# Optimization experiments

Hardware: AMD Instinct MI355X
Metric: run time of the kernel (lower is better)

The kernel has to match this reference:

```python
import jax, jax.numpy as jnp
import numpy as np

D_MODEL = 1024
NHEAD = 16
HEAD_DIM = D_MODEL // NHEAD
ROPE_BASE = 10000.0


def _rope_freq(T, head_dim):
    half = head_dim // 2
    pos = jnp.arange(T, dtype=jnp.float32)
    idx = jnp.arange(half, dtype=jnp.float32)
    freq_div = ROPE_BASE ** (2.0 * idx / head_dim)
    return pos[:, None] / freq_div[None, :]  # [T, half]


def _rope_rotate(x, cos, sin):
    # x: [B, H, T, d]; cos/sin: [T, d//2]
    half = x.shape[-1] // 2
    xl, xr = x[..., :half], x[..., half:]
    c = cos[None, None]
    s = sin[None, None]
    return jnp.concatenate([xl * c - xr * s, xl * s + xr * c], axis=-1)


def setup_inputs() -> dict:
    key = jax.random.key(0)
    ks = jax.random.split(key, 12)
    B, T = 2, 2048
    sd = 1.0 / np.sqrt(D_MODEL)
    inp = {
        "query": jax.random.normal(ks[0], (B, T, D_MODEL), jnp.float32),
        "key": jax.random.normal(ks[1], (B, T, D_MODEL), jnp.float32),
        "value": jax.random.normal(ks[2], (B, T, D_MODEL), jnp.float32),
        "frac": jax.random.uniform(ks[3], (B, T), jnp.float32),
        # Linear weights stored [in, out] (torch W.T)
        "Wq": jax.random.normal(ks[4], (D_MODEL, D_MODEL), jnp.float32) * sd,
        "Wk": jax.random.normal(ks[5], (D_MODEL, D_MODEL), jnp.float32) * sd,
        "Wv": jax.random.normal(ks[6], (D_MODEL, D_MODEL), jnp.float32) * sd,
        "Wo": jax.random.normal(ks[7], (D_MODEL, D_MODEL), jnp.float32) * sd,
        "bq": jnp.zeros((D_MODEL,), jnp.float32),
        "bk": jnp.zeros((D_MODEL,), jnp.float32),
        "bv": jnp.zeros((D_MODEL,), jnp.float32),
        "bo": jnp.zeros((D_MODEL,), jnp.float32),
        "alpha_pos": jax.random.normal(ks[8], (NHEAD,), jnp.float32) * 0.1,
        "alpha_neg": jax.random.normal(ks[9], (NHEAD,), jnp.float32) * 0.1,
    }
    return inp


def reference(query, key, value, frac, Wq, Wk, Wv, Wo, bq, bk, bv, bo, alpha_pos, alpha_neg):
    B, T, dm = query.shape
    H, hd = NHEAD, HEAD_DIM
    scale = hd ** -0.5

    def split_heads(x):  # [B,T,dm] -> [B,H,T,hd]
        return x.reshape(B, T, H, hd).transpose(0, 2, 1, 3)

    Q = split_heads(query @ Wq + bq)
    K = split_heads(key @ Wk + bk)
    V = split_heads(value @ Wv + bv)

    freq = _rope_freq(T, hd)
    cos, sin = jnp.cos(freq), jnp.sin(freq)
    Q = _rope_rotate(Q, cos, sin)
    K = _rope_rotate(K, cos, sin)

    scores = jnp.einsum("bhqd,bhkd->bhqk", Q, K) * scale  # [B,H,T,T]

    # data-dependent stoichiometric bias
    D = frac[:, None, :] - frac[:, :, None]  # [B,T,T], D[b,i,j] = frac_j - frac_i
    D_pos = jax.nn.relu(D)
    D_neg = -jax.nn.relu(-D)
    bias = (alpha_pos[None, :, None, None] * D_pos[:, None] +
            alpha_neg[None, :, None, None] * D_neg[:, None])  # [B,H,T,T]
    scores = scores + bias

    probs = jax.nn.softmax(scores, axis=-1)
    out = jnp.einsum("bhqk,bhkd->bhqd", probs, V)  # [B,H,T,hd]
    out = out.transpose(0, 2, 1, 3).reshape(B, T, dm)
    return out @ Wo + bo
```

## Files before the change

kernel.cpp:

```cpp
#include <hip/hip_runtime.h>


typedef unsigned short u16;
typedef __bf16 bf8v __attribute__((ext_vector_type(8)));
typedef __bf16 bf4v __attribute__((ext_vector_type(4)));
typedef float f32x4 __attribute__((ext_vector_type(4)));

#define D_MODEL 1024
#define T_SEQ   2048
#define NHEAD   16
#define HDIM    64
#define BATCH   2
#define M_TOT   (BATCH * T_SEQ)
#define LOG2E   1.4426950408889634f

__device__ __forceinline__ void gl2lds16(const u16* g, u16* l) {
  __builtin_amdgcn_global_load_lds(
      (__attribute__((address_space(1))) void*)g,
      (__attribute__((address_space(3))) void*)l, 16, 0, 0);
}

__global__ __launch_bounds__(256) void k_prep(
    const float* __restrict__ q, const float* __restrict__ k,
    const float* __restrict__ v, const float* __restrict__ Wq,
    const float* __restrict__ Wk, const float* __restrict__ Wv,
    const float* __restrict__ Wo, u16* __restrict__ Xb, u16* __restrict__ WtB,
    float* __restrict__ ct, float* __restrict__ st) {
  __shared__ float tile[64 * 65];
  int bx = blockIdx.x, tid = threadIdx.x;
  if (bx < 6144) {
    int z = bx >> 11, xb = bx & 2047;
    const float* src = (z == 0) ? q : (z == 1) ? k : v;
    u16* dst = Xb + (size_t)z * (M_TOT * D_MODEL);
    int idx = (xb * 256 + tid) * 8;
    float4 a = *(const float4*)(src + idx);
    float4 b = *(const float4*)(src + idx + 4);
    bf8v o;
    o[0] = (__bf16)a.x; o[1] = (__bf16)a.y; o[2] = (__bf16)a.z; o[3] = (__bf16)a.w;
    o[4] = (__bf16)b.x; o[5] = (__bf16)b.y; o[6] = (__bf16)b.z; o[7] = (__bf16)b.w;
    *(bf8v*)(dst + idx) = o;
  } else if (bx < 7168) {
    int idx2 = bx - 6144;
    int z = idx2 >> 8, rem = idx2 & 255;
    int k0 = (rem >> 4) * 64, n0 = (rem & 15) * 64;
    const float* W = (z == 0) ? Wq : (z == 1) ? Wk : (z == 2) ? Wv : Wo;
    u16* Wt = WtB + (size_t)z * (D_MODEL * D_MODEL);
#pragma unroll
    for (int i = 0; i < 16; i++) {
      int idx = tid + i * 256;
      int r = idx >> 6, c = idx & 63;
      tile[c * 65 + r] = W[(size_t)(k0 + r) * D_MODEL + n0 + c];
    }
    __syncthreads();
#pragma unroll
    for (int i = 0; i < 16; i++) {
      int idx = tid + i * 256;
      int r = idx >> 6, c = idx & 63;
      ((__bf16*)Wt)[(size_t)(n0 + r) * D_MODEL + k0 + c] = (__bf16)tile[r * 65 + c];
    }
  } else {
    int idx = (bx - 7168) * 256 + tid;
    int t = idx >> 5, d = idx & 31;
    float ang = (float)t * powf(10000.0f, -(float)d * (1.0f / 32.0f));
    ct[idx] = cosf(ang);
    st[idx] = sinf(ang);
  }
}

__device__ __forceinline__ void gemm_core_128(const u16* __restrict__ A,
                                              const u16* __restrict__ Bt,
                                              u16* sA, u16* sB,
                                              f32x4 (&acc)[4][4],
                                              int m0, int n0) {
  const int K = D_MODEL;
  int tid = threadIdx.x;
  int lane = tid & 63, wave = tid >> 6;
  int l15 = lane & 15, quad = lane >> 4;
  int wm = (wave >> 1) * 64, wn = (wave & 1) * 64;
  int r0 = tid >> 2, pcol0 = (tid & 3) * 8;
  int r1 = 64 + r0;
  const u16* A0 = A + (size_t)(m0 + r0) * K + pcol0;
  const u16* A1 = A + (size_t)(m0 + r1) * K + pcol0;
  const u16* B0 = Bt + (size_t)(n0 + r0) * K + pcol0;
  const u16* B1 = Bt + (size_t)(n0 + r1) * K + pcol0;
  u16* dA0 = sA + wave * 512;
  u16* dA1 = sA + 2048 + wave * 512;
  u16* dB0 = sB + wave * 512;
  u16* dB1 = sB + 2048 + wave * 512;
  for (int k0 = 0; k0 < K; k0 += 64) {
    __syncthreads();
    gl2lds16(A0 + k0, dA0);
    gl2lds16(A1 + k0, dA1);
    gl2lds16(A0 + k0 + 32, dA0 + 4096);
    gl2lds16(A1 + k0 + 32, dA1 + 4096);
    gl2lds16(B0 + k0, dB0);
    gl2lds16(B0 + k0 + 32, dB0 + 4096);
    gl2lds16(B1 + k0, dB1);
    gl2lds16(B1 + k0 + 32, dB1 + 4096);
    __syncthreads();
#pragma unroll
    for (int kh = 0; kh < 2; kh++) {
      bf8v af[4], bf[4];
#pragma unroll
      for (int i = 0; i < 4; i++)
        af[i] = *(const bf8v*)(sA + kh * 4096 + (wm + i * 16 + l15) * 32 + quad * 8);
#pragma unroll
      for (int i = 0; i < 4; i++)
        bf[i] = *(const bf8v*)(sB + kh * 4096 + (wn + i * 16 + l15) * 32 + quad * 8);
#pragma unroll
      for (int mi = 0; mi < 4; mi++)
#pragma unroll
        for (int ni = 0; ni < 4; ni++)
          acc[mi][ni] = __builtin_amdgcn_mfma_f32_16x16x32_bf16(
              af[mi], bf[ni], acc[mi][ni], 0, 0, 0);
    }
  }
}

__global__ __launch_bounds__(256) void k_gemm_qkv(
    const u16* __restrict__ Xb, const u16* __restrict__ WtB,
    const float* __restrict__ bq, const float* __restrict__ bk,
    const float* __restrict__ bv, const float* __restrict__ ctab,
    const float* __restrict__ stab, u16* __restrict__ OutB,
    u16* __restrict__ Vb) {
  __shared__ __align__(16) u16 sA[128 * 64];
  __shared__ __align__(16) u16 sB[128 * 64];
  int z = blockIdx.z;
  const u16* A = Xb + (size_t)z * (M_TOT * D_MODEL);
  const u16* Bt = WtB + (size_t)z * (D_MODEL * D_MODEL);
  const float* bias = (z == 0) ? bq : (z == 1) ? bk : bv;
  u16* Out = OutB + (size_t)z * (M_TOT * D_MODEL);
  int m0 = blockIdx.y * 128, n0 = blockIdx.x * 128;
  f32x4 acc[4][4] = {};
  gemm_core_128(A, Bt, sA, sB, acc, m0, n0);

  int tid = threadIdx.x, lane = tid & 63, wave = tid >> 6;
  int l15 = lane & 15, quad = lane >> 4;
  int wm = (wave >> 1) * 64, wn = (wave & 1) * 64;
  float bvv[4];
#pragma unroll
  for (int ni = 0; ni < 4; ni++) bvv[ni] = bias[n0 + wn + ni * 16 + l15];

  if (z < 2) {
    float qs = (z == 0) ? 0.125f * LOG2E : 1.0f;
#pragma unroll
    for (int mi = 0; mi < 4; mi++) {
#pragma unroll
      for (int r = 0; r < 4; r++) {
        int m = m0 + wm + mi * 16 + quad * 4 + r;
        size_t ro = (size_t)m * D_MODEL + n0 + wn;
        int tl = m & (T_SEQ - 1);
#pragma unroll
        for (int ni = 0; ni < 2; ni++) {
          int d = ni * 16 + l15;
          float c = ctab[tl * 32 + d], s = stab[tl * 32 + d];
          float xl = acc[mi][ni][r] + bvv[ni];
          float xr = acc[mi][ni + 2][r] + bvv[ni + 2];
          ((__bf16*)Out)[ro + d] = (__bf16)((xl * c - xr * s) * qs);
          ((__bf16*)Out)[ro + d + 32] = (__bf16)((xl * s + xr * c) * qs);
        }
      }
    }
  } else {
    int hh = (n0 + wn) >> 6;
    int mbase = m0 + wm;
    int bb = mbase >> 11;
    int tbase = mbase & (T_SEQ - 1);
    u16* Vw = Vb + (size_t)(bb * NHEAD + hh) * HDIM * T_SEQ;
#pragma unroll
    for (int mi = 0; mi < 4; mi++)
#pragma unroll
      for (int r = 0; r < 4; r++) {
        int t = tbase + mi * 16 + quad * 4 + r;
#pragma unroll
        for (int ni = 0; ni < 4; ni++) {
          int d = ni * 16 + l15;
          ((__bf16*)Vw)[(size_t)d * T_SEQ + t] = (__bf16)(acc[mi][ni][r] + bvv[ni]);
        }
      }
  }
}

__global__ __launch_bounds__(256) void k_gemm_out(
    const u16* __restrict__ ctx, const u16* __restrict__ Wot,
    const float* __restrict__ bo, float* __restrict__ Cout) {
  __shared__ __align__(16) u16 sA[64 * 64];
  __shared__ __align__(16) u16 sB[64 * 64];
  const int K = D_MODEL;
  int m0 = blockIdx.y * 64, n0 = blockIdx.x * 64;
  int tid = threadIdx.x, lane = tid & 63, wave = tid >> 6;
  int l15 = lane & 15, quad = lane >> 4;
  int wm = (wave >> 1) * 32, wn = (wave & 1) * 32;
  int r0 = tid >> 2, pcol0 = (tid & 3) * 8;
  const u16* A0 = ctx + (size_t)(m0 + r0) * K + pcol0;
  const u16* B0 = Wot + (size_t)(n0 + r0) * K + pcol0;
  u16* dA = sA + wave * 512;
  u16* dB = sB + wave * 512;
  f32x4 acc[2][2] = {};
  for (int k0 = 0; k0 < K; k0 += 64) {
    __syncthreads();
    gl2lds16(A0 + k0, dA);
    gl2lds16(A0 + k0 + 32, dA + 2048);
    gl2lds16(B0 + k0, dB);
    gl2lds16(B0 + k0 + 32, dB + 2048);
    __syncthreads();
#pragma unroll
    for (int kh = 0; kh < 2; kh++) {
      bf8v af[2], bf[2];
#pragma unroll
      for (int i = 0; i < 2; i++)
        af[i] = *(const bf8v*)(sA + kh * 2048 + (wm + i * 16 + l15) * 32 + quad * 8);
#pragma unroll
      for (int i = 0; i < 2; i++)
        bf[i] = *(const bf8v*)(sB + kh * 2048 + (wn + i * 16 + l15) * 32 + quad * 8);
#pragma unroll
      for (int mi = 0; mi < 2; mi++)
#pragma unroll
        for (int ni = 0; ni < 2; ni++)
          acc[mi][ni] = __builtin_amdgcn_mfma_f32_16x16x32_bf16(
              af[mi], bf[ni], acc[mi][ni], 0, 0, 0);
    }
  }
  float bvv[2];
#pragma unroll
  for (int ni = 0; ni < 2; ni++) bvv[ni] = bo[n0 + wn + ni * 16 + l15];
#pragma unroll
  for (int mi = 0; mi < 2; mi++)
#pragma unroll
    for (int r = 0; r < 4; r++) {
      size_t ro = (size_t)(m0 + wm + mi * 16 + quad * 4 + r) * D_MODEL + n0 + wn;
#pragma unroll
      for (int ni = 0; ni < 2; ni++)
        Cout[ro + ni * 16 + l15] = acc[mi][ni][r] + bvv[ni];
    }
}

__global__ __launch_bounds__(256) void k_attn(
    const u16* __restrict__ Qr, const u16* __restrict__ Kr,
    const u16* __restrict__ Vb, const float* __restrict__ frac,
    const float* __restrict__ alpha_pos, const float* __restrict__ alpha_neg,
    u16* __restrict__ ctx) {
  __shared__ __align__(16) u16 kT[2][64 * 64];
  __shared__ __align__(16) u16 vT[2][64 * 64];
  __shared__ __align__(16) u16 pT[4][2][16 * 72];
  int bh = blockIdx.y, b = bh >> 4, h = bh & 15;
  int q0 = blockIdx.x * 128;
  int tid = threadIdx.x, wave = tid >> 6, lane = tid & 63;
  int l15 = lane & 15, quad = lane >> 4;

  const u16* Kh = Kr + (size_t)b * T_SEQ * D_MODEL + h * HDIM;
  const u16* Vh = Vb + (size_t)bh * HDIM * T_SEQ;
  const float* fb = frac + b * T_SEQ;

  bf8v qf[2][2];
  float fq[2];
#pragma unroll
  for (int g = 0; g < 2; g++) {
    int qrow = q0 + wave * 32 + g * 16 + l15;
    const u16* qbase =
        Qr + (size_t)(b * T_SEQ + qrow) * D_MODEL + h * HDIM + quad * 8;
    qf[g][0] = *(const bf8v*)qbase;
    qf[g][1] = *(const bf8v*)(qbase + 32);
    fq[g] = fb[qrow];
  }
  float ap = alpha_pos[h] * LOG2E, an = alpha_neg[h] * LOG2E;
  bf8v onesv;
#pragma unroll
  for (int j = 0; j < 8; j++) onesv[j] = (__bf16)1.0f;
  f32x4 o[2][4] = {};
  f32x4 o_l[2] = {};
  u16* pw = &pT[wave][0][0];

  int x0 = (quad ^ (l15 & 7)) * 8;
  int kidx[4], vidx[4];
#pragma unroll
  for (int nt = 0; nt < 4; nt++) kidx[nt] = ((nt * 16 + l15) << 6) + x0;
#pragma unroll
  for (int dt = 0; dt < 4; dt++) vidx[dt] = ((dt * 16 + l15) << 6) + x0;
  int pidx = l15 * 72 + quad * 8;

  int p0 = tid, p1 = 256 + tid;
  int kr0 = p0 >> 3, gc0 = (p0 & 7) ^ (kr0 & 7);
  int kr1 = p1 >> 3, gc1 = (p1 & 7) ^ (kr1 & 7);
  const u16* kg0 = Kh + (size_t)kr0 * D_MODEL + gc0 * 8;
  const u16* kg1 = Kh + (size_t)kr1 * D_MODEL + gc1 * 8;
  const u16* vg0 = Vh + (size_t)kr0 * T_SEQ + gc0 * 8;
  const u16* vg1 = Vh + (size_t)kr1 * T_SEQ + gc1 * 8;
  int woff = wave * 512;

  auto stage = [&](int buf, int kbase) {
    gl2lds16(kg0 + (size_t)kbase * D_MODEL, kT[buf] + woff);
    gl2lds16(kg1 + (size_t)kbase * D_MODEL, kT[buf] + 2048 + woff);
    gl2lds16(vg0 + kbase, vT[buf] + woff);
    gl2lds16(vg1 + kbase, vT[buf] + 2048 + woff);
  };

  stage(0, 0);
  __syncthreads();

  for (int kt = 0; kt < T_SEQ / 64; kt++) {
    int kbase = kt * 64;
    int buf = kt & 1;
    if (kt + 1 < T_SEQ / 64) stage(buf ^ 1, kbase + 64);
    const u16* kb = kT[buf];
    const u16* vb = vT[buf];

    bf8v kf0[4], kf1[4];
#pragma unroll
    for (int nt = 0; nt < 4; nt++) {
      kf0[nt] = *(const bf8v*)(kb + kidx[nt]);
      kf1[nt] = *(const bf8v*)(kb + (kidx[nt] ^ 32));
    }
    bf8v vf[2][4];
#pragma unroll
    for (int dt = 0; dt < 4; dt++) {
      vf[0][dt] = *(const bf8v*)(vb + vidx[dt]);
      vf[1][dt] = *(const bf8v*)(vb + (vidx[dt] ^ 32));
    }
    f32x4 fk4[4];
#pragma unroll
    for (int nt = 0; nt < 4; nt++)
      fk4[nt] = *(const f32x4*)(fb + kbase + nt * 16 + quad * 4);

#pragma unroll
    for (int g = 0; g < 2; g++) {
      float fqg = fq[g];
      u16* pwg = pw + g * (16 * 72);
#pragma unroll
      for (int nt = 0; nt < 4; nt++) {
        f32x4 s = {};
        s = __builtin_amdgcn_mfma_f32_16x16x32_bf16(kf0[nt], qf[g][0], s, 0, 0, 0);
        s = __builtin_amdgcn_mfma_f32_16x16x32_bf16(kf1[nt], qf[g][1], s, 0, 0, 0);
        bf4v pk;
#pragma unroll
        for (int r = 0; r < 4; r++) {
          float dd = fk4[nt][r] - fqg;
          float sel = (dd >= 0.0f) ? ap : an;
          pk[r] = (__bf16)__builtin_amdgcn_exp2f(fmaf(dd, sel, s[r]));
        }
        *(bf4v*)(pwg + l15 * 72 + nt * 16 + quad * 4) = pk;
      }
      asm volatile("s_waitcnt lgkmcnt(0)" ::: "memory");
#pragma unroll
      for (int kc = 0; kc < 2; kc++) {
        bf8v pf = *(const bf8v*)(pwg + pidx + kc * 32);
        o_l[g] = __builtin_amdgcn_mfma_f32_16x16x32_bf16(pf, onesv, o_l[g], 0, 0, 0);
#pragma unroll
        for (int dt = 0; dt < 4; dt++)
          o[g][dt] = __builtin_amdgcn_mfma_f32_16x16x32_bf16(pf, vf[kc][dt],
                                                             o[g][dt], 0, 0, 0);
      }
    }
    __syncthreads();
  }

#pragma unroll
  for (int g = 0; g < 2; g++) {
#pragma unroll
    for (int r = 0; r < 4; r++) {
      float linv = 1.0f / o_l[g][r];
      int qg = q0 + wave * 32 + g * 16 + quad * 4 + r;
      __bf16* orow = (__bf16*)(ctx + (size_t)(b * T_SEQ + qg) * D_MODEL + h * HDIM);
#pragma unroll
      for (int dt = 0; dt < 4; dt++)
        orow[dt * 16 + l15] = (__bf16)(o[g][dt][r] * linv);
    }
  }
}

extern "C" void kernel_launch(void* const* d_in, const int* in_sizes, int n_in,
                              void* d_out, int out_size, void* d_ws,
                              size_t ws_size, hipStream_t stream) {
  const float* q = (const float*)d_in[0];
  const float* k = (const float*)d_in[1];
  const float* v = (const float*)d_in[2];
  const float* frac = (const float*)d_in[3];
  const float* Wq = (const float*)d_in[4];
  const float* Wk = (const float*)d_in[5];
  const float* Wv = (const float*)d_in[6];
  const float* Wo = (const float*)d_in[7];
  const float* bq = (const float*)d_in[8];
  const float* bk = (const float*)d_in[9];
  const float* bv = (const float*)d_in[10];
  const float* bo = (const float*)d_in[11];
  const float* alpha_pos = (const float*)d_in[12];
  const float* alpha_neg = (const float*)d_in[13];

  char* ws = (char*)d_ws;
  u16* Xb = (u16*)(ws + 0);
  u16* Wt = (u16*)(ws + 25165824);
  u16* Qr = (u16*)(ws + 33554432);
  u16* Kr = (u16*)(ws + 41943040);
  u16* Vtmp = (u16*)(ws + 50331648);
  u16* Vb = (u16*)(ws + 58720256);
  float* ctab = (float*)(ws + 67108864);
  float* stab = (float*)(ws + 67371008);
  u16* ctx = Vtmp;
  u16* QKVout = Qr;

  k_prep<<<dim3(7424), 256, 0, stream>>>(q, k, v, Wq, Wk, Wv, Wo, Xb, Wt, ctab,
                                         stab);
  k_gemm_qkv<<<dim3(8, 32, 3), 256, 0, stream>>>(Xb, Wt, bq, bk, bv, ctab, stab,
                                                 QKVout, Vb);
  k_attn<<<dim3(16, 32), 256, 0, stream>>>(Qr, Kr, Vb, frac, alpha_pos,
                                           alpha_neg, ctx);
  k_gemm_out<<<dim3(16, 64), 256, 0, stream>>>(ctx, Wt + 3 * 1048576, bo,
                                               (float*)d_out);
}
```

Baseline: 256.1 us.

## Split attention key tiles across two wave groups and merge partial outputs

The attention kernel grows from 256 to 512 threads. Each group of four waves handles half of every 64-key tile for the same 128 queries, so each wave does half the score and PV work per tile and staging is spread across more threads. Partial numerators and row sums are merged through shared memory at the end. The piecewise bias select is also replaced by an abs-based form (c1*d + c2*|d|). This adds a final reduction, a sync and more LDS use, and launch_bounds(512,4) may limit registers.

```diff
diff --git a/kernel.cpp b/kernel.cpp
--- a/kernel.cpp
+++ b/kernel.cpp
@@ -235,18 +235,18 @@
     }
 }
 
-__global__ __launch_bounds__(256) void k_attn(
+__global__ __launch_bounds__(512, 4) void k_attn(
     const u16* __restrict__ Qr, const u16* __restrict__ Kr,
     const u16* __restrict__ Vb, const float* __restrict__ frac,
     const float* __restrict__ alpha_pos, const float* __restrict__ alpha_neg,
     u16* __restrict__ ctx) {
-  __shared__ __align__(16) u16 kT[2][64 * 64];
-  __shared__ __align__(16) u16 vT[2][64 * 64];
-  __shared__ __align__(16) u16 pT[4][2][16 * 72];
+  __shared__ __align__(16) u16 smem[26624];
   int bh = blockIdx.y, b = bh >> 4, h = bh & 15;
   int q0 = blockIdx.x * 128;
   int tid = threadIdx.x, wave = tid >> 6, lane = tid & 63;
   int l15 = lane & 15, quad = lane >> 4;
+  int qw = wave & 3;
+  int kh = wave >> 2;
 
   const u16* Kh = Kr + (size_t)b * T_SEQ * D_MODEL + h * HDIM;
   const u16* Vh = Vb + (size_t)bh * HDIM * T_SEQ;
@@ -256,7 +256,7 @@
   float fq[2];
 #pragma unroll
   for (int g = 0; g < 2; g++) {
-    int qrow = q0 + wave * 32 + g * 16 + l15;
+    int qrow = q0 + qw * 32 + g * 16 + l15;
     const u16* qbase =
         Qr + (size_t)(b * T_SEQ + qrow) * D_MODEL + h * HDIM + quad * 8;
     qf[g][0] = *(const bf8v*)qbase;
@@ -264,35 +264,34 @@
     fq[g] = fb[qrow];
   }
   float ap = alpha_pos[h] * LOG2E, an = alpha_neg[h] * LOG2E;
+  float c1 = 0.5f * (ap + an), c2 = 0.5f * (ap - an);
   bf8v onesv;
 #pragma unroll
   for (int j = 0; j < 8; j++) onesv[j] = (__bf16)1.0f;
   f32x4 o[2][4] = {};
   f32x4 o_l[2] = {};
-  u16* pw = &pT[wave][0][0];
+  u16* kT0 = smem;
+  u16* vT0 = smem + 8192;
+  u16* pw = smem + 16384 + wave * 1280;
 
   int x0 = (quad ^ (l15 & 7)) * 8;
-  int kidx[4], vidx[4];
-#pragma unroll
-  for (int nt = 0; nt < 4; nt++) kidx[nt] = ((nt * 16 + l15) << 6) + x0;
-#pragma unroll
-  for (int dt = 0; dt < 4; dt++) vidx[dt] = ((dt * 16 + l15) << 6) + x0;
-  int pidx = l15 * 72 + quad * 8;
-
-  int p0 = tid, p1 = 256 + tid;
-  int kr0 = p0 >> 3, gc0 = (p0 & 7) ^ (kr0 & 7);
-  int kr1 = p1 >> 3, gc1 = (p1 & 7) ^ (kr1 & 7);
+  int kidx[2], vidx[4];
+#pragma unroll
+  for (int nt = 0; nt < 2; nt++)
+    kidx[nt] = (((kh * 2 + nt) * 16 + l15) << 6) + x0;
+#pragma unroll
+  for (int dt = 0; dt < 4; dt++)
+    vidx[dt] = (((dt * 16 + l15) << 6) + x0) ^ (kh * 32);
+  int pidx = l15 * 40 + quad * 8;
+
+  int kr0 = tid >> 3, gc0 = (tid & 7) ^ (kr0 & 7);
   const u16* kg0 = Kh + (size_t)kr0 * D_MODEL + gc0 * 8;
-  const u16* kg1 = Kh + (size_t)kr1 * D_MODEL + gc1 * 8;
   const u16* vg0 = Vh + (size_t)kr0 * T_SEQ + gc0 * 8;
-  const u16* vg1 = Vh + (size_t)kr1 * T_SEQ + gc1 * 8;
   int woff = wave * 512;
 
   auto stage = [&](int buf, int kbase) {
-    gl2lds16(kg0 + (size_t)kbase * D_MODEL, kT[buf] + woff);
-    gl2lds16(kg1 + (size_t)kbase * D_MODEL, kT[buf] + 2048 + woff);
-    gl2lds16(vg0 + kbase, vT[buf] + woff);
-    gl2lds16(vg1 + kbase, vT[buf] + 2048 + woff);
+    gl2lds16(kg0 + (size_t)kbase * D_MODEL, kT0 + buf * 4096 + woff);
+    gl2lds16(vg0 + kbase, vT0 + buf * 4096 + woff);
   };
 
   stage(0, 0);
@@ -302,32 +301,29 @@
     int kbase = kt * 64;
     int buf = kt & 1;
     if (kt + 1 < T_SEQ / 64) stage(buf ^ 1, kbase + 64);
-    const u16* kb = kT[buf];
-    const u16* vb = vT[buf];
-
-    bf8v kf0[4], kf1[4];
-#pragma unroll
-    for (int nt = 0; nt < 4; nt++) {
+    const u16* kb = kT0 + buf * 4096;
+    const u16* vb = vT0 + buf * 4096;
+
+    bf8v kf0[2], kf1[2];
+#pragma unroll
+    for (int nt = 0; nt < 2; nt++) {
       kf0[nt] = *(const bf8v*)(kb + kidx[nt]);
       kf1[nt] = *(const bf8v*)(kb + (kidx[nt] ^ 32));
     }
-    bf8v vf[2][4];
-#pragma unroll
-    for (int dt = 0; dt < 4; dt++) {
-      vf[0][dt] = *(const bf8v*)(vb + vidx[dt]);
-      vf[1][dt] = *(const bf8v*)(vb + (vidx[dt] ^ 32));
-    }
-    f32x4 fk4[4];
-#pragma unroll
-    for (int nt = 0; nt < 4; nt++)
-      fk4[nt] = *(const f32x4*)(fb + kbase + nt * 16 + quad * 4);
+    bf8v vf[4];
+#pragma unroll
+    for (int dt = 0; dt < 4; dt++) vf[dt] = *(const bf8v*)(vb + vidx[dt]);
+    f32x4 fk4[2];
+#pragma unroll
+    for (int nt = 0; nt < 2; nt++)
+      fk4[nt] = *(const f32x4*)(fb + kbase + kh * 32 + nt * 16 + quad * 4);
 
 #pragma unroll
     for (int g = 0; g < 2; g++) {
       float fqg = fq[g];
-      u16* pwg = pw + g * (16 * 72);
-#pragma unroll
-      for (int nt = 0; nt < 4; nt++) {
+      u16* pwg = pw + g * 640;
+#pragma unroll
+      for (int nt = 0; nt < 2; nt++) {
         f32x4 s = {};
         s = __builtin_amdgcn_mfma_f32_16x16x32_bf16(kf0[nt], qf[g][0], s, 0, 0, 0);
         s = __builtin_amdgcn_mfma_f32_16x16x32_bf16(kf1[nt], qf[g][1], s, 0, 0, 0);
@@ -335,36 +331,51 @@
 #pragma unroll
         for (int r = 0; r < 4; r++) {
           float dd = fk4[nt][r] - fqg;
-          float sel = (dd >= 0.0f) ? ap : an;
-          pk[r] = (__bf16)__builtin_amdgcn_exp2f(fmaf(dd, sel, s[r]));
+          pk[r] = (__bf16)__builtin_amdgcn_exp2f(
+              fmaf(c2, __builtin_fabsf(dd), fmaf(c1, dd, s[r])));
         }
-        *(bf4v*)(pwg + l15 * 72 + nt * 16 + quad * 4) = pk;
+        *(bf4v*)(pwg + l15 * 40 + nt * 16 + quad * 4) = pk;
       }
       asm volatile("s_waitcnt lgkmcnt(0)" ::: "memory");
-#pragma unroll
-      for (int kc = 0; kc < 2; kc++) {
-        bf8v pf = *(const bf8v*)(pwg + pidx + kc * 32);
-        o_l[g] = __builtin_amdgcn_mfma_f32_16x16x32_bf16(pf, onesv, o_l[g], 0, 0, 0);
+      bf8v pf = *(const bf8v*)(pwg + pidx);
+      o_l[g] = __builtin_amdgcn_mfma_f32_16x16x32_bf16(pf, onesv, o_l[g], 0, 0, 0);
+#pragma unroll
+      for (int dt = 0; dt < 4; dt++)
+        o[g][dt] = __builtin_amdgcn_mfma_f32_16x16x32_bf16(pf, vf[dt],
+                                                           o[g][dt], 0, 0, 0);
+    }
+    __syncthreads();
+  }
+
+  float* Of = (float*)smem;
+  float* Lf = (float*)(smem + 26368);
+  if (kh == 1) {
+#pragma unroll
+    for (int g = 0; g < 2; g++)
+#pragma unroll
+      for (int r = 0; r < 4; r++) {
+        int ql = qw * 32 + g * 16 + quad * 4 + r;
 #pragma unroll
         for (int dt = 0; dt < 4; dt++)
-          o[g][dt] = __builtin_amdgcn_mfma_f32_16x16x32_bf16(pf, vf[kc][dt],
-                                                             o[g][dt], 0, 0, 0);
+          Of[ql * 66 + dt * 16 + l15] = o[g][dt][r];
+        if (l15 == 0) Lf[ql] = o_l[g][r];
       }
-    }
-    __syncthreads();
-  }
-
-#pragma unroll
-  for (int g = 0; g < 2; g++) {
-#pragma unroll
-    for (int r = 0; r < 4; r++) {
-      float linv = 1.0f / o_l[g][r];
-      int qg = q0 + wave * 32 + g * 16 + quad * 4 + r;
-      __bf16* orow = (__bf16*)(ctx + (size_t)(b * T_SEQ + qg) * D_MODEL + h * HDIM);
-#pragma unroll
-      for (int dt = 0; dt < 4; dt++)
-        orow[dt * 16 + l15] = (__bf16)(o[g][dt][r] * linv);
-    }
+  }
+  __syncthreads();
+  if (kh == 0) {
+#pragma unroll
+    for (int g = 0; g < 2; g++)
+#pragma unroll
+      for (int r = 0; r < 4; r++) {
+        int ql = qw * 32 + g * 16 + quad * 4 + r;
+        float linv = 1.0f / (o_l[g][r] + Lf[ql]);
+        __bf16* orow =
+            (__bf16*)(ctx + (size_t)(b * T_SEQ + q0 + ql) * D_MODEL + h * HDIM);
+#pragma unroll
+        for (int dt = 0; dt < 4; dt++)
+          orow[dt * 16 + l15] =
+              (__bf16)((o[g][dt][r] + Of[ql * 66 + dt * 16 + l15]) * linv);
+      }
   }
 }
 
@@ -402,7 +413,7 @@
                                          stab);
   k_gemm_qkv<<<dim3(8, 32, 3), 256, 0, stream>>>(Xb, Wt, bq, bk, bv, ctab, stab,
                                                  QKVout, Vb);
-  k_attn<<<dim3(16, 32), 256, 0, stream>>>(Qr, Kr, Vb, frac, alpha_pos,
+  k_attn<<<dim3(16, 32), 512, 0, stream>>>(Qr, Kr, Vb, frac, alpha_pos,
                                            alpha_neg, ctx);
   k_gemm_out<<<dim3(16, 64), 256, 0, stream>>>(ctx, Wt + 3 * 1048576, bo,
                                                (float*)d_out);
```

After: 240.0 us. 6.3% less time.
